# Kernel optimization log

Hardware: AMD Instinct MI355X
Metric: run time of the kernel (lower is better)

The kernel has to match this reference:

```python
import jax, jax.numpy as jnp
import numpy as np

N_NODES = 100_000
N_EDGES = 600_000
D = 128  # in_channels


def setup_inputs() -> dict:
    key = jax.random.key(0)
    k1, k2, k3, k4, k5 = jax.random.split(key, 5)
    node_embs_src = jax.random.normal(k1, (N_NODES, D), dtype=jnp.float32)
    node_embs_dst = jax.random.normal(k2, (N_NODES, D), dtype=jnp.float32)
    edge_index = jax.random.randint(k3, (2, N_EDGES), 0, N_NODES, dtype=jnp.int64)
    # MLP params: Linear(2D -> D), Linear(D -> 1); scaled like default torch init
    W1 = jax.random.normal(k4, (2 * D, D), dtype=jnp.float32) / np.sqrt(2 * D)
    b1 = jnp.zeros((D,), dtype=jnp.float32)
    W2 = jax.random.normal(k5, (D, 1), dtype=jnp.float32) / np.sqrt(D)
    b2 = jnp.zeros((1,), dtype=jnp.float32)
    return {
        "node_embs_src": node_embs_src,
        "node_embs_dst": node_embs_dst,
        "edge_index": edge_index,
        "W1": W1,
        "b1": b1,
        "W2": W2,
        "b2": b2,
    }


def reference(node_embs_src, node_embs_dst, edge_index, W1, b1, W2, b2):
    # Gather per-edge source / destination embeddings: [E, D] each
    src = node_embs_src[edge_index[0]]
    dst = node_embs_dst[edge_index[1]]
    # concat([src, dst]) @ W1 == src @ W1[:D] + dst @ W1[D:]  (avoids materializing [E, 2D])
    h = jnp.dot(src, W1[:D]) + jnp.dot(dst, W1[D:]) + b1  # [E, D]
    h = jax.nn.relu(h)
    logits = jnp.dot(h, W2) + b2  # [E, 1]
    return jax.nn.sigmoid(logits)
```

## Files before the change

kernel.cpp:

```cpp
#include <hip/hip_runtime.h>
#include <stdint.h>

typedef __attribute__((ext_vector_type(8))) short short8;
typedef __attribute__((ext_vector_type(8))) signed char schar8;
typedef __attribute__((ext_vector_type(4))) float f32x4;

__device__ __forceinline__ unsigned short f2bf(float f) {
  union { float f; uint32_t u; } v; v.f = f;
  uint32_t u = v.u;
  uint32_t r = (u + 0x7FFFu + ((u >> 16) & 1u)) >> 16;
  return (unsigned short)r;
}
__device__ __forceinline__ float bf2f(unsigned short h) {
  union { uint32_t u; float f; } v; v.u = ((uint32_t)h) << 16; return v.f;
}

#define NBM 64
__global__ __launch_bounds__(256, 4)
void node_phase_bf16(const float* __restrict__ src_emb,
                     const float* __restrict__ dst_emb,
                     const float* __restrict__ W1,
                     const float* __restrict__ b1,
                     unsigned short* __restrict__ UV,
                     int Nn, int ntiles) {
  __shared__ __align__(16) char Als[NBM * 256];

  const int tbl = blockIdx.y;
  const float* emb = tbl ? dst_emb : src_emb;
  const float* Wt  = W1 + (size_t)tbl * 128 * 128;
  unsigned short* outp = UV + (size_t)tbl * Nn * 128;

  const int tid  = threadIdx.x;
  const int lane = tid & 63;
  const int w    = tid >> 6;
  const int l15  = lane & 15;
  const int lk8  = (lane >> 4) * 8;

  short8 bfrag[4][2];
#pragma unroll
  for (int s = 0; s < 4; ++s) {
#pragma unroll
    for (int nf = 0; nf < 2; ++nf) {
      const int col = w * 32 + 2 * l15 + nf;
      short8 t;
#pragma unroll
      for (int j = 0; j < 8; ++j) {
        const int k = s * 32 + lk8 + j;
        t[j] = (short)f2bf(Wt[k * 128 + col]);
      }
      bfrag[s][nf] = t;
    }
  }
  const int colb = w * 32 + 2 * l15;
  const float bias0 = tbl ? 0.f : b1[colb];
  const float bias1 = tbl ? 0.f : b1[colb + 1];

  const int q = tid & 15, r0 = tid >> 4;
  const int swz = (l15 & 7) << 4;
  const int gx = gridDim.x;

  float4 p0[4], p1[4];
#pragma unroll
  for (int i = 0; i < 4; ++i) {
    const int node = blockIdx.x * NBM + i * 16 + r0;
    if (node < Nn) {
      const float* base = emb + (size_t)node * 128 + q * 8;
      p0[i] = *(const float4*)base;
      p1[i] = *(const float4*)(base + 4);
    }
  }

  for (int t = blockIdx.x; t < ntiles; t += gx) {
    const int t0 = t * NBM;

#pragma unroll
    for (int i = 0; i < 4; ++i) {
      const int row = i * 16 + r0;
      short8 hv;
      hv[0] = (short)f2bf(p0[i].x); hv[1] = (short)f2bf(p0[i].y);
      hv[2] = (short)f2bf(p0[i].z); hv[3] = (short)f2bf(p0[i].w);
      hv[4] = (short)f2bf(p1[i].x); hv[5] = (short)f2bf(p1[i].y);
      hv[6] = (short)f2bf(p1[i].z); hv[7] = (short)f2bf(p1[i].w);
      const int byteoff = row * 256 + ((q * 16) ^ ((row & 7) << 4));
      *(short8*)(Als + byteoff) = hv;
    }
    __syncthreads();

    const int tn = t + gx;
    if (tn < ntiles) {
#pragma unroll
      for (int i = 0; i < 4; ++i) {
        const int node = tn * NBM + i * 16 + r0;
        if (node < Nn) {
          const float* base = emb + (size_t)node * 128 + q * 8;
          p0[i] = *(const float4*)base;
          p1[i] = *(const float4*)(base + 4);
        }
      }
    }

#pragma unroll
    for (int m = 0; m < 4; ++m) {
      f32x4 acc0 = {0.f, 0.f, 0.f, 0.f};
      f32x4 acc1 = {0.f, 0.f, 0.f, 0.f};
      const int rowb = (m * 16 + l15) * 256;
      const int kb0  = lk8 * 2;
#pragma unroll
      for (int s = 0; s < 4; ++s) {
        const int off = rowb + ((s * 64 + kb0) ^ swz);
        const short8 a = *(const short8*)(Als + off);
        acc0 = __builtin_amdgcn_mfma_f32_16x16x32_bf16(a, bfrag[s][0], acc0, 0, 0, 0);
        acc1 = __builtin_amdgcn_mfma_f32_16x16x32_bf16(a, bfrag[s][1], acc1, 0, 0, 0);
      }
#pragma unroll
      for (int reg = 0; reg < 4; ++reg) {
        const int orow = t0 + m * 16 + ((lane >> 4) * 4) + reg;
        if (orow < Nn) {
          const uint32_t pk = (uint32_t)f2bf(acc0[reg] + bias0) |
                              ((uint32_t)f2bf(acc1[reg] + bias1) << 16);
          *(uint32_t*)&outp[(size_t)orow * 128 + colb] = pk;
        }
      }
    }
    __syncthreads();
  }
}

__global__ __launch_bounds__(256, 8)
void quant_rows_q8(const unsigned short* __restrict__ UV,
                   int8_t* __restrict__ Q,
                   float* __restrict__ SC,
                   int nrows) {
  const int tid = threadIdx.x;
  const int l15 = tid & 15;
  const int stride = gridDim.x * 16;

  for (int r = blockIdx.x * 16 + (tid >> 4); r < nrows; r += stride) {
    const short8 v = *(const short8*)(UV + (size_t)r * 128 + l15 * 8);
    float f[8];
    float am = 1e-20f;
#pragma unroll
    for (int j = 0; j < 8; ++j) {
      f[j] = bf2f((unsigned short)v[j]);
      am = fmaxf(am, fabsf(f[j]));
    }
    am = fmaxf(am, __shfl_xor(am, 1, 16));
    am = fmaxf(am, __shfl_xor(am, 2, 16));
    am = fmaxf(am, __shfl_xor(am, 4, 16));
    am = fmaxf(am, __shfl_xor(am, 8, 16));
    const float rq = 127.0f / am;
    uint32_t lo = 0, hi = 0;
#pragma unroll
    for (int j = 0; j < 4; ++j)
      lo |= ((uint32_t)((int)rintf(f[j] * rq) & 255)) << (8 * j);
#pragma unroll
    for (int j = 4; j < 8; ++j)
      hi |= ((uint32_t)((int)rintf(f[j] * rq) & 255)) << (8 * (j - 4));
    uint2 pk; pk.x = lo; pk.y = hi;
    *(uint2*)(Q + (size_t)r * 128 + l15 * 8) = pk;
    if (l15 == 0) SC[r] = am * (1.0f / 127.0f);
  }
}

__global__ __launch_bounds__(256, 8)
void edge_phase_q8(const int8_t* __restrict__ Qu,
                   const int8_t* __restrict__ Qv,
                   const float* __restrict__ scu,
                   const float* __restrict__ scv,
                   const int* __restrict__ eidx,
                   const float* __restrict__ W2,
                   const float* __restrict__ b2,
                   float* __restrict__ out,
                   int E) {
  const int tid = threadIdx.x;
  const int l15 = tid & 15;
  const int sg  = tid >> 4;

  float w2s[8];
#pragma unroll
  for (int j = 0; j < 8; ++j) w2s[j] = W2[l15 * 8 + j];
  const float b2s = b2[0];
  const int stride = gridDim.x * 16;

#pragma unroll 2
  for (int e = blockIdx.x * 16 + sg; e < E; e += stride) {
    const int s = eidx[e];
    const int d = eidx[E + e];
    const schar8 qu = *(const schar8*)(Qu + (size_t)s * 128 + l15 * 8);
    const schar8 qv = *(const schar8*)(Qv + (size_t)d * 128 + l15 * 8);
    const float su = scu[s];
    const float sv = scv[d];
    float acc = 0.f;
#pragma unroll
    for (int j = 0; j < 8; ++j) {
      float g = (float)(int)qu[j] * su + (float)(int)qv[j] * sv;
      g = g > 0.f ? g : 0.f;
      acc = fmaf(g, w2s[j], acc);
    }
    acc += __shfl_xor(acc, 1, 16);
    acc += __shfl_xor(acc, 2, 16);
    acc += __shfl_xor(acc, 4, 16);
    acc += __shfl_xor(acc, 8, 16);
    if (l15 == 0) out[e] = 1.f / (1.f + __expf(-(acc + b2s)));
  }
}

__global__ __launch_bounds__(256, 8)
void edge_phase_bf16(const unsigned short* __restrict__ UV,
                     const int* __restrict__ eidx,
                     const float* __restrict__ W2,
                     const float* __restrict__ b2,
                     float* __restrict__ out,
                     int E, int Nn) {
  const int tid = threadIdx.x;
  const int l15 = tid & 15;
  const int sg  = tid >> 4;

  float w2s[8];
#pragma unroll
  for (int j = 0; j < 8; ++j) w2s[j] = W2[l15 * 8 + j];
  const float b2s = b2[0];
  const unsigned short* U = UV;
  const unsigned short* V = UV + (size_t)Nn * 128;
  const int stride = gridDim.x * 16;

#pragma unroll 2
  for (int e = blockIdx.x * 16 + sg; e < E; e += stride) {
    const int s = eidx[e];
    const int d = eidx[E + e];
    const short8 u8 = *(const short8*)(U + (size_t)s * 128 + l15 * 8);
    const short8 v8 = *(const short8*)(V + (size_t)d * 128 + l15 * 8);
    float acc = 0.f;
#pragma unroll
    for (int j = 0; j < 8; ++j) {
      float g = bf2f((unsigned short)u8[j]) + bf2f((unsigned short)v8[j]);
      g = g > 0.f ? g : 0.f;
      acc = fmaf(g, w2s[j], acc);
    }
    acc += __shfl_xor(acc, 1, 16);
    acc += __shfl_xor(acc, 2, 16);
    acc += __shfl_xor(acc, 4, 16);
    acc += __shfl_xor(acc, 8, 16);
    if (l15 == 0) out[e] = 1.f / (1.f + __expf(-(acc + b2s)));
  }
}

#define BM 64
__global__ __launch_bounds__(256, 4)
void edge_decoder_fused(const float* __restrict__ src_emb,
                        const float* __restrict__ dst_emb,
                        const int* __restrict__ eidx,
                        const float* __restrict__ W1,
                        const float* __restrict__ b1,
                        const float* __restrict__ W2,
                        const float* __restrict__ b2,
                        float* __restrict__ out,
                        int E, int ntiles) {
  __shared__ __align__(16) char Als[BM * 512];
  __shared__ float rowpart[4][BM];

  const int tid  = threadIdx.x;
  const int lane = tid & 63;
  const int w    = tid >> 6;
  const int l15  = lane & 15;
  const int lk8  = (lane >> 4) * 8;

  short8 bfrag[8][2];
#pragma unroll
  for (int s = 0; s < 8; ++s) {
#pragma unroll
    for (int nf = 0; nf < 2; ++nf) {
      const int col = w * 32 + nf * 16 + l15;
      short8 t;
#pragma unroll
      for (int j = 0; j < 8; ++j) {
        const int k = s * 32 + lk8 + j;
        t[j] = (short)f2bf(W1[k * 128 + col]);
      }
      bfrag[s][nf] = t;
    }
  }
  float b1v[2], w2v[2];
#pragma unroll
  for (int nf = 0; nf < 2; ++nf) {
    const int col = w * 32 + nf * 16 + l15;
    b1v[nf] = b1[col];
    w2v[nf] = W2[col];
  }
  const float b2s = b2[0];

  const int q  = tid & 31;
  const int r0 = tid >> 5;
  const int qq = q & 15;
  const bool is_src = (q < 16);
  const int swz = (l15 & 7) << 4;

  for (int t = blockIdx.x; t < ntiles; t += gridDim.x) {
    const int t0 = t * BM;
#pragma unroll
    for (int i = 0; i < 8; ++i) {
      const int row = i * 8 + r0;
      const int e = t0 + row;
      if (e < E) {
        const int node = is_src ? eidx[e] : eidx[E + e];
        const float* base = (is_src ? src_emb : dst_emb) + (size_t)node * 128 + qq * 8;
        const float4 f0 = *(const float4*)base;
        const float4 f1 = *(const float4*)(base + 4);
        short8 hv;
        hv[0] = (short)f2bf(f0.x); hv[1] = (short)f2bf(f0.y);
        hv[2] = (short)f2bf(f0.z); hv[3] = (short)f2bf(f0.w);
        hv[4] = (short)f2bf(f1.x); hv[5] = (short)f2bf(f1.y);
        hv[6] = (short)f2bf(f1.z); hv[7] = (short)f2bf(f1.w);
        const int byteoff = row * 512 + ((q * 16) ^ ((row & 7) << 4));
        *(short8*)(Als + byteoff) = hv;
      }
    }
    __syncthreads();

    for (int m = 0; m < 4; ++m) {
      f32x4 acc0 = {0.f, 0.f, 0.f, 0.f};
      f32x4 acc1 = {0.f, 0.f, 0.f, 0.f};
      const int rowb = (m * 16 + l15) * 512;
      const int kb0  = lk8 * 2;
#pragma unroll
      for (int s = 0; s < 8; ++s) {
        const int off = rowb + ((s * 64 + kb0) ^ swz);
        const short8 a = *(const short8*)(Als + off);
        acc0 = __builtin_amdgcn_mfma_f32_16x16x32_bf16(a, bfrag[s][0], acc0, 0, 0, 0);
        acc1 = __builtin_amdgcn_mfma_f32_16x16x32_bf16(a, bfrag[s][1], acc1, 0, 0, 0);
      }
      float pr[4];
#pragma unroll
      for (int reg = 0; reg < 4; ++reg) {
        float h0 = acc0[reg] + b1v[0]; h0 = h0 > 0.f ? h0 : 0.f;
        float h1 = acc1[reg] + b1v[1]; h1 = h1 > 0.f ? h1 : 0.f;
        pr[reg] = h0 * w2v[0] + h1 * w2v[1];
      }
#pragma unroll
      for (int off = 1; off < 16; off <<= 1) {
#pragma unroll
        for (int reg = 0; reg < 4; ++reg)
          pr[reg] += __shfl_xor(pr[reg], off, 64);
      }
      if (l15 == 0) {
        const int rbase = m * 16 + (lane >> 4) * 4;
#pragma unroll
        for (int reg = 0; reg < 4; ++reg)
          rowpart[w][rbase + reg] = pr[reg];
      }
    }
    __syncthreads();

    if (tid < BM) {
      const int e = t0 + tid;
      if (e < E) {
        const float sum = rowpart[0][tid] + rowpart[1][tid] +
                          rowpart[2][tid] + rowpart[3][tid] + b2s;
        out[e] = 1.f / (1.f + __expf(-sum));
      }
    }
    __syncthreads();
  }
}

extern "C" void kernel_launch(void* const* d_in, const int* in_sizes, int n_in,
                              void* d_out, int out_size, void* d_ws, size_t ws_size,
                              hipStream_t stream) {
  const float* src = (const float*)d_in[0];
  const float* dst = (const float*)d_in[1];
  const int*   eix = (const int*)d_in[2];
  const float* W1  = (const float*)d_in[3];
  const float* b1  = (const float*)d_in[4];
  const float* W2  = (const float*)d_in[5];
  const float* b2  = (const float*)d_in[6];
  float* out = (float*)d_out;

  const int E  = in_sizes[2] / 2;
  const int Nn = in_sizes[0] / 128;
  const int nrows = 2 * Nn;
  const size_t uv_bytes = (size_t)nrows * 128 * 2;
  const size_t q_bytes  = (size_t)nrows * 128;
  const size_t sc_bytes = (size_t)nrows * sizeof(float);

  const int ntiles_n = (Nn + NBM - 1) / NBM;
  const int gx = ntiles_n < 1024 ? ntiles_n : 1024;
  const int nchunks = (E + 15) / 16;
  const int nblk = nchunks < 2048 ? nchunks : 2048;

  if (ws_size >= uv_bytes + q_bytes + sc_bytes) {
    unsigned short* UV = (unsigned short*)d_ws;
    int8_t* Q  = (int8_t*)((char*)d_ws + uv_bytes);
    float*  SC = (float*)((char*)d_ws + uv_bytes + q_bytes);
    node_phase_bf16<<<dim3(gx, 2), 256, 0, stream>>>(src, dst, W1, b1, UV, Nn, ntiles_n);
    const int qblk = ((nrows + 15) / 16) < 2048 ? ((nrows + 15) / 16) : 2048;
    quant_rows_q8<<<qblk, 256, 0, stream>>>(UV, Q, SC, nrows);
    edge_phase_q8<<<nblk, 256, 0, stream>>>(Q, Q + (size_t)Nn * 128, SC, SC + Nn,
                                            eix, W2, b2, out, E);
  } else if (ws_size >= uv_bytes) {
    unsigned short* UV = (unsigned short*)d_ws;
    node_phase_bf16<<<dim3(gx, 2), 256, 0, stream>>>(src, dst, W1, b1, UV, Nn, ntiles_n);
    edge_phase_bf16<<<nblk, 256, 0, stream>>>(UV, eix, W2, b2, out, E, Nn);
  } else {
    const int ntiles = (E + BM - 1) / BM;
    const int grid = ntiles < 2048 ? ntiles : 2048;
    edge_decoder_fused<<<grid, 256, 0, stream>>>(src, dst, eix, W1, b1, W2, b2,
                                                 out, E, ntiles);
  }
}
```

Baseline: 74.33 us.

## Stage node embeddings via direct global-to-LDS loads and convert to bf16 at MFMA time

The node-phase GEMM now copies fp32 embedding rows straight into shared memory with global_load_lds (swizzled source addresses) instead of loading into registers, converting to bf16, and storing to LDS. Conversion to bf16 moves to the MFMA operand read and uses truncation rather than round-to-nearest. The register-level prefetch of the next tile is removed and the grid cap drops from 1024 to 640 blocks. This cuts register traffic and VALU conversion work but doubles LDS footprint, gives up the software prefetch overlap, and slightly changes rounding.

```diff
diff --git a/kernel.cpp b/kernel.cpp
--- a/kernel.cpp
+++ b/kernel.cpp
@@ -13,6 +13,16 @@
 }
 __device__ __forceinline__ float bf2f(unsigned short h) {
   union { uint32_t u; float f; } v; v.u = ((uint32_t)h) << 16; return v.f;
+}
+__device__ __forceinline__ uint32_t pkbf(float a, float b) {
+  union { float f; uint32_t u; } x, y; x.f = a; y.f = b;
+  return (x.u >> 16) | (y.u & 0xFFFF0000u);
+}
+__device__ __forceinline__ void gload_lds16(const void* g, void* l) {
+  __builtin_amdgcn_global_load_lds(
+      (const __attribute__((address_space(1))) void*)g,
+      (__attribute__((address_space(3))) void*)l,
+      16, 0, 0);
 }
 
 #define NBM 64
@@ -23,7 +33,7 @@
                      const float* __restrict__ b1,
                      unsigned short* __restrict__ UV,
                      int Nn, int ntiles) {
-  __shared__ __align__(16) char Als[NBM * 256];
+  __shared__ __align__(16) float Als[NBM * 128];
 
   const int tbl = blockIdx.y;
   const float* emb = tbl ? dst_emb : src_emb;
@@ -34,7 +44,8 @@
   const int lane = tid & 63;
   const int w    = tid >> 6;
   const int l15  = lane & 15;
-  const int lk8  = (lane >> 4) * 8;
+  const int lg   = lane >> 4;
+  const int lk8  = lg * 8;
 
   short8 bfrag[4][2];
 #pragma unroll
@@ -55,66 +66,45 @@
   const float bias0 = tbl ? 0.f : b1[colb];
   const float bias1 = tbl ? 0.f : b1[colb + 1];
 
-  const int q = tid & 15, r0 = tid >> 4;
-  const int swz = (l15 & 7) << 4;
+  const int jhalf = lane >> 5;
+  const int cb    = (lane & 31) * 16;
+  char* ldsw = (char*)Als + w * 8192;
   const int gx = gridDim.x;
-
-  float4 p0[4], p1[4];
-#pragma unroll
-  for (int i = 0; i < 4; ++i) {
-    const int node = blockIdx.x * NBM + i * 16 + r0;
-    if (node < Nn) {
-      const float* base = emb + (size_t)node * 128 + q * 8;
-      p0[i] = *(const float4*)base;
-      p1[i] = *(const float4*)(base + 4);
-    }
-  }
+  const int swzA = (l15 & 7) << 4;
 
   for (int t = blockIdx.x; t < ntiles; t += gx) {
     const int t0 = t * NBM;
 
 #pragma unroll
-    for (int i = 0; i < 4; ++i) {
-      const int row = i * 16 + r0;
-      short8 hv;
-      hv[0] = (short)f2bf(p0[i].x); hv[1] = (short)f2bf(p0[i].y);
-      hv[2] = (short)f2bf(p0[i].z); hv[3] = (short)f2bf(p0[i].w);
-      hv[4] = (short)f2bf(p1[i].x); hv[5] = (short)f2bf(p1[i].y);
-      hv[6] = (short)f2bf(p1[i].z); hv[7] = (short)f2bf(p1[i].w);
-      const int byteoff = row * 256 + ((q * 16) ^ ((row & 7) << 4));
-      *(short8*)(Als + byteoff) = hv;
-    }
-    __syncthreads();
-
-    const int tn = t + gx;
-    if (tn < ntiles) {
-#pragma unroll
-      for (int i = 0; i < 4; ++i) {
-        const int node = tn * NBM + i * 16 + r0;
-        if (node < Nn) {
-          const float* base = emb + (size_t)node * 128 + q * 8;
-          p0[i] = *(const float4*)base;
-          p1[i] = *(const float4*)(base + 4);
-        }
-      }
-    }
+    for (int j = 0; j < 8; ++j) {
+      const int row = w * 16 + 2 * j + jhalf;
+      int node = t0 + row; node = node < Nn ? node : Nn - 1;
+      const char* src = (const char*)(emb + (size_t)node * 128)
+                        + (cb ^ ((row & 7) << 4));
+      gload_lds16(src, ldsw + j * 1024 + lane * 16);
+    }
+    __syncthreads();
 
 #pragma unroll
     for (int m = 0; m < 4; ++m) {
       f32x4 acc0 = {0.f, 0.f, 0.f, 0.f};
       f32x4 acc1 = {0.f, 0.f, 0.f, 0.f};
-      const int rowb = (m * 16 + l15) * 256;
-      const int kb0  = lk8 * 2;
+      const int rbase = (m * 16 + l15) * 512;
 #pragma unroll
       for (int s = 0; s < 4; ++s) {
-        const int off = rowb + ((s * 64 + kb0) ^ swz);
-        const short8 a = *(const short8*)(Als + off);
+        const int kb = s * 128 + lg * 32;
+        const float4 fa = *(const float4*)((const char*)Als + rbase + (kb ^ swzA));
+        const float4 fb = *(const float4*)((const char*)Als + rbase + ((kb + 16) ^ swzA));
+        short8 a;
+        uint32_t* au = (uint32_t*)&a;
+        au[0] = pkbf(fa.x, fa.y); au[1] = pkbf(fa.z, fa.w);
+        au[2] = pkbf(fb.x, fb.y); au[3] = pkbf(fb.z, fb.w);
         acc0 = __builtin_amdgcn_mfma_f32_16x16x32_bf16(a, bfrag[s][0], acc0, 0, 0, 0);
         acc1 = __builtin_amdgcn_mfma_f32_16x16x32_bf16(a, bfrag[s][1], acc1, 0, 0, 0);
       }
 #pragma unroll
       for (int reg = 0; reg < 4; ++reg) {
-        const int orow = t0 + m * 16 + ((lane >> 4) * 4) + reg;
+        const int orow = t0 + m * 16 + lg * 4 + reg;
         if (orow < Nn) {
           const uint32_t pk = (uint32_t)f2bf(acc0[reg] + bias0) |
                               ((uint32_t)f2bf(acc1[reg] + bias1) << 16);
@@ -383,7 +373,7 @@
   const size_t sc_bytes = (size_t)nrows * sizeof(float);
 
   const int ntiles_n = (Nn + NBM - 1) / NBM;
-  const int gx = ntiles_n < 1024 ? ntiles_n : 1024;
+  const int gx = ntiles_n < 640 ? ntiles_n : 640;
   const int nchunks = (E + 15) / 16;
   const int nblk = nchunks < 2048 ? nchunks : 2048;
 
```

Result: slower. 76.22 us (+2.5%).
